# Performance work log

Hardware: AMD Instinct MI355X
Metric: run time of the kernel (lower is better)

## Reference

```python
import jax, jax.numpy as jnp
import numpy as np

USER_NUM = 100000
ITEM_NUM = 100000
N_NODES = USER_NUM + ITEM_NUM
EMB = 64
N_EDGES = 6400000
N_LAYERS = 3
LAYER_CL = 1
EPS = 0.1


def setup_inputs() -> dict:
    key = jax.random.key(0)
    k1, k2, k3, k4, k5, k6 = jax.random.split(key, 6)
    # Xavier-uniform-like scale for embeddings
    scale = float(np.sqrt(6.0 / (USER_NUM + EMB)))
    user_emb = jax.random.normal(k1, (USER_NUM, EMB), dtype=jnp.float32) * scale
    item_emb = jax.random.normal(k2, (ITEM_NUM, EMB), dtype=jnp.float32) * scale
    adj_rows = jax.random.randint(k3, (N_EDGES,), 0, N_NODES, dtype=jnp.int64)
    adj_cols = jax.random.randint(k4, (N_EDGES,), 0, N_NODES, dtype=jnp.int64)
    # normalized adjacency values ~ 1/degree
    adj_vals = jax.random.uniform(k5, (N_EDGES,), dtype=jnp.float32) * (1.0 / 32.0)
    # precomputed uniform noise replacing torch.rand_like per layer
    noise = jax.random.uniform(k6, (N_LAYERS, N_NODES, EMB), dtype=jnp.float32)
    return {"user_emb": user_emb, "item_emb": item_emb, "adj_rows": adj_rows,
            "adj_cols": adj_cols, "adj_vals": adj_vals, "noise": noise}


def _spmm(rows, cols, vals, x):
    # sparse [N,N] @ dense [N,D] via gather + segment_sum
    return jax.ops.segment_sum(vals[:, None] * x[cols], rows, num_segments=N_NODES)


def reference(user_emb, item_emb, adj_rows, adj_cols, adj_vals, noise):
    ego = jnp.concatenate([user_emb, item_emb], axis=0)  # [N, D]
    cl = ego
    acc = jnp.zeros_like(ego)
    for k in range(N_LAYERS):
        ego = _spmm(adj_rows, adj_cols, adj_vals, ego)
        # perturbed branch: ego += sign(ego) * F.normalize(noise_k, dim=-1) * eps
        nk = noise[k]
        nrm = jnp.maximum(jnp.linalg.norm(nk, axis=-1, keepdims=True), 1e-12)
        ego = ego + jnp.sign(ego) * (nk / nrm) * EPS
        acc = acc + ego
        if k == LAYER_CL - 1:
            cl = ego
    final = acc / N_LAYERS  # mean over stacked layer outputs
    return (final[:USER_NUM], final[USER_NUM:], cl[:USER_NUM], cl[USER_NUM:])
```

## Files before the change

kernel.cpp:

```cpp
#include <hip/hip_runtime.h>


#define USER_NUM 100000
#define N_NODES  200000
#define EMB      64
#define N_EDGES  6400000
#define NBUCK    782
#define CAP      9216
#define EPB      16384
#define TB_A     1024

static constexpr size_t BUFA_OFF  = 0;
static constexpr size_t BUFB_OFF  = 51200000;
static constexpr size_t CV_OFF    = 102400000;
static constexpr size_t RS_OFF    = 153600000;
static constexpr size_t SMALL_OFF = 154400016;
static constexpr size_t NRM_OFF   = 155200016;
static constexpr size_t WS_NEED   = 156000016;

__global__ __launch_bounds__(TB_A) void k_prep(const int* __restrict__ rows,
                                               const int* __restrict__ cols,
                                               const float* __restrict__ vals,
                                               int* __restrict__ bcnt,
                                               int2* __restrict__ zip) {
    __shared__ int h[NBUCK];
    for (int i = threadIdx.x; i < NBUCK; i += TB_A) h[i] = 0;
    __syncthreads();
    int base = blockIdx.x * EPB;
    int end  = min(base + EPB, N_EDGES);
    for (int e = base + threadIdx.x; e < end; e += TB_A) {
        atomicAdd(&h[rows[e] >> 8], 1);
        zip[e] = make_int2(cols[e], __float_as_int(vals[e]));
    }
    __syncthreads();
    for (int i = threadIdx.x; i < NBUCK; i += TB_A) {
        int c = h[i];
        if (c) atomicAdd(&bcnt[i], c);
    }
}

__global__ void k_scan782(const int* __restrict__ bcnt, int* __restrict__ bbase,
                          int* __restrict__ gcur, int* __restrict__ rs) {
    __shared__ int s[1024];
    int i = threadIdx.x;
    int v = (i < NBUCK) ? bcnt[i] : 0;
    s[i] = v;
    __syncthreads();
    for (int off = 1; off < 1024; off <<= 1) {
        int t = 0;
        if (i >= off) t = s[i - off];
        __syncthreads();
        s[i] += t;
        __syncthreads();
    }
    if (i < NBUCK) {
        int ex = s[i] - v;
        bbase[i] = ex;
        gcur[i] = ex;
    }
    if (i == 0) rs[N_NODES] = N_EDGES;
}

__global__ __launch_bounds__(TB_A) void k_bin(const int* __restrict__ rows,
                                              int* __restrict__ gcur,
                                              int* __restrict__ keys) {
    __shared__ int h[NBUCK];
    __shared__ int gb[NBUCK];
    for (int i = threadIdx.x; i < NBUCK; i += TB_A) h[i] = 0;
    __syncthreads();
    int base = blockIdx.x * EPB;
    int end  = min(base + EPB, N_EDGES);
    for (int e = base + threadIdx.x; e < end; e += TB_A)
        atomicAdd(&h[rows[e] >> 8], 1);
    __syncthreads();
    for (int i = threadIdx.x; i < NBUCK; i += TB_A) {
        int c = h[i];
        gb[i] = c ? atomicAdd(&gcur[i], c) : 0;
        h[i] = 0;
    }
    __syncthreads();
    for (int e = base + threadIdx.x; e < end; e += TB_A) {
        int r = rows[e];
        int b = r >> 8;
        int pos = gb[b] + atomicAdd(&h[b], 1);
        keys[pos] = ((r & 255) << 24) | e;
    }
}

__global__ __launch_bounds__(256) void k_build(const int* __restrict__ keys,
                                               const int2* __restrict__ zip,
                                               const int* __restrict__ bcnt,
                                               const int* __restrict__ bbase,
                                               int2* __restrict__ cv,
                                               int* __restrict__ rs) {
    __shared__ int cnt[256];
    __shared__ int start[256];
    __shared__ int cur[256];
    __shared__ int scanbuf[256];
    __shared__ int eKey[CAP];
    int tid = threadIdx.x;
    int b = blockIdx.x;
    int n = bcnt[b];
    int base = bbase[b];
    int rowbase = b << 8;
    cnt[tid] = 0;
    __syncthreads();
    for (int i = tid; i < n; i += 256) {
        unsigned key = (unsigned)keys[base + i];
        atomicAdd(&cnt[key >> 24], 1);
    }
    __syncthreads();
    int v = cnt[tid];
    scanbuf[tid] = v;
    __syncthreads();
    for (int off = 1; off < 256; off <<= 1) {
        int t = 0;
        if (tid >= off) t = scanbuf[tid - off];
        __syncthreads();
        scanbuf[tid] += t;
        __syncthreads();
    }
    start[tid] = scanbuf[tid] - v;
    {
        int row = rowbase + tid;
        if (row < N_NODES) rs[row] = base + start[tid];
    }
    cur[tid] = 0;
    __syncthreads();
    if (n <= CAP) {
        for (int i = tid; i < n; i += 256) {
            int key = keys[base + i];
            int rl = (int)((unsigned)key >> 24);
            int p = start[rl] + atomicAdd(&cur[rl], 1);
            eKey[p] = key;
        }
        __syncthreads();
        for (int p = tid; p < n; p += 256) {
            int k = eKey[p];
            int rl = (int)((unsigned)k >> 24);
            int s0 = start[rl];
            int s1 = s0 + cnt[rl];
            int rank = 0;
            int q = s0;
            for (; q + 4 <= s1; q += 4) {
                rank += (eKey[q]     < k);
                rank += (eKey[q + 1] < k);
                rank += (eKey[q + 2] < k);
                rank += (eKey[q + 3] < k);
            }
            for (; q < s1; ++q) rank += (eKey[q] < k);
            int e = k & 0x00FFFFFF;
            cv[base + s0 + rank] = zip[e];
        }
    } else {
        for (int i = tid; i < n; i += 256) {
            int key = keys[base + i];
            int rl = (int)((unsigned)key >> 24);
            int p = start[rl] + atomicAdd(&cur[rl], 1);
            cv[base + p] = make_int2(key, 0);
        }
        __syncthreads();
        int c = cnt[tid];
        if (c > 1) {
            int s0 = start[tid];
            int s1 = s0 + c;
            for (int i = s0 + 1; i < s1; ++i) {
                int2 kv = cv[base + i];
                int j = i - 1;
                while (j >= s0 && cv[base + j].x > kv.x) {
                    cv[base + j + 1] = cv[base + j];
                    --j;
                }
                cv[base + j + 1] = kv;
            }
        }
        __syncthreads();
        for (int i = tid; i < n; i += 256) {
            int e = cv[base + i].x & 0x00FFFFFF;
            cv[base + i] = zip[e];
        }
    }
}

__global__ void k_norm(const float* __restrict__ nk, float* __restrict__ nrm) {
    __shared__ float tile[2][64 * 65];
    int wave = threadIdx.x >> 6;
    int lane = threadIdx.x & 63;
    int base = blockIdx.x * 128 + wave * 64;
    for (int rr = 0; rr < 64; ++rr) {
        int row = base + rr;
        float v = 0.f;
        if (row < N_NODES) v = nk[row * EMB + lane];
        tile[wave][rr * 65 + lane] = v;
    }
    __syncthreads();
    int row = base + lane;
    if (row < N_NODES) {
        const float* tp = &tile[wave][lane * 65];
        float rj[8];
        #pragma unroll
        for (int j = 0; j < 8; ++j) {
            float xj = tp[j];
            rj[j] = __fmul_rn(xj, xj);
        }
        #pragma unroll
        for (int i = 8; i < 64; i += 8) {
            #pragma unroll
            for (int j = 0; j < 8; ++j) {
                float xj = tp[i + j];
                rj[j] = __fadd_rn(rj[j], __fmul_rn(xj, xj));
            }
        }
        float s01 = __fadd_rn(rj[0], rj[1]);
        float s23 = __fadd_rn(rj[2], rj[3]);
        float s45 = __fadd_rn(rj[4], rj[5]);
        float s67 = __fadd_rn(rj[6], rj[7]);
        float ss = __fadd_rn(__fadd_rn(s01, s23), __fadd_rn(s45, s67));
        float nv = __fsqrt_rn(ss);
        nv = fmaxf(nv, 1e-12f);
        nrm[row] = nv;
    }
}

__global__ __launch_bounds__(256) void k_fused(const int* __restrict__ rs,
                                               const int2* __restrict__ cv,
                                               const float* __restrict__ xlo,
                                               const float* __restrict__ xhi,
                                               int split,
                                               const float* __restrict__ nk,
                                               const float* __restrict__ nrm,
                                               float* __restrict__ ego,
                                               float* __restrict__ accF,
                                               float* __restrict__ clF,
                                               int mode) {
    int t = blockIdx.x * blockDim.x + threadIdx.x;
    if (t >= N_NODES * 16) return;
    int r = t >> 4;
    int c = (t & 15) << 2;
    int j0 = rs[r], j1 = rs[r + 1];
    float a0 = 0.f, a1 = 0.f, a2 = 0.f, a3 = 0.f;
    if (j0 < j1) {
        const int EMAX = N_EDGES - 1;
        #define XROW(col) (((col) < split ? xlo : xhi) + \
                           ((col) < split ? (col) : (col) - split) * EMB + c)
        int2 c0 = cv[j0];
        int2 c1 = cv[min(j0 + 1, EMAX)];
        int2 c2 = cv[min(j0 + 2, EMAX)];
        int2 n0 = cv[min(j0 + 3, EMAX)];
        int2 n1 = cv[min(j0 + 4, EMAX)];
        int2 n2 = cv[min(j0 + 5, EMAX)];
        int2 m0 = cv[min(j0 + 6, EMAX)];
        int2 m1 = cv[min(j0 + 7, EMAX)];
        int2 m2 = cv[min(j0 + 8, EMAX)];
        float4 x0 = *(const float4*)XROW(c0.x);
        float4 x1 = *(const float4*)XROW(c1.x);
        float4 x2 = *(const float4*)XROW(c2.x);
        for (int j = j0; j < j1; j += 3) {
            float4 y0 = *(const float4*)XROW(n0.x);
            float4 y1 = *(const float4*)XROW(n1.x);
            float4 y2 = *(const float4*)XROW(n2.x);
            float v0 = __int_as_float(c0.y);
            float v1 = (j + 1 < j1) ? __int_as_float(c1.y) : 0.f;
            float v2 = (j + 2 < j1) ? __int_as_float(c2.y) : 0.f;
            a0 = __fadd_rn(a0, __fmul_rn(v0, x0.x));
            a1 = __fadd_rn(a1, __fmul_rn(v0, x0.y));
            a2 = __fadd_rn(a2, __fmul_rn(v0, x0.z));
            a3 = __fadd_rn(a3, __fmul_rn(v0, x0.w));
            a0 = __fadd_rn(a0, __fmul_rn(v1, x1.x));
            a1 = __fadd_rn(a1, __fmul_rn(v1, x1.y));
            a2 = __fadd_rn(a2, __fmul_rn(v1, x1.z));
            a3 = __fadd_rn(a3, __fmul_rn(v1, x1.w));
            a0 = __fadd_rn(a0, __fmul_rn(v2, x2.x));
            a1 = __fadd_rn(a1, __fmul_rn(v2, x2.y));
            a2 = __fadd_rn(a2, __fmul_rn(v2, x2.z));
            a3 = __fadd_rn(a3, __fmul_rn(v2, x2.w));
            c0 = n0; c1 = n1; c2 = n2;
            n0 = m0; n1 = m1; n2 = m2;
            x0 = y0; x1 = y1; x2 = y2;
            m0 = cv[min(j + 9,  EMAX)];
            m1 = cv[min(j + 10, EMAX)];
            m2 = cv[min(j + 11, EMAX)];
        }
        #undef XROW
    }
    int idx = t << 2;
    float4 n4 = *(const float4*)(nk + idx);
    float nv = nrm[r];
    float4 e4;
    {
        float s, q;
        s = (a0 > 0.f) ? 1.f : ((a0 < 0.f) ? -1.f : 0.f);
        q = __fdiv_rn(n4.x, nv);
        e4.x = __fadd_rn(a0, __fmul_rn(__fmul_rn(s, q), 0.1f));
        s = (a1 > 0.f) ? 1.f : ((a1 < 0.f) ? -1.f : 0.f);
        q = __fdiv_rn(n4.y, nv);
        e4.y = __fadd_rn(a1, __fmul_rn(__fmul_rn(s, q), 0.1f));
        s = (a2 > 0.f) ? 1.f : ((a2 < 0.f) ? -1.f : 0.f);
        q = __fdiv_rn(n4.z, nv);
        e4.z = __fadd_rn(a2, __fmul_rn(__fmul_rn(s, q), 0.1f));
        s = (a3 > 0.f) ? 1.f : ((a3 < 0.f) ? -1.f : 0.f);
        q = __fdiv_rn(n4.w, nv);
        e4.w = __fadd_rn(a3, __fmul_rn(__fmul_rn(s, q), 0.1f));
    }
    if (mode == 0) {
        *(float4*)(ego + idx) = e4;
        *(float4*)(clF + idx) = e4;
    } else if (mode == 1) {
        *(float4*)(ego + idx) = e4;
        float4 a = *(const float4*)(clF + idx);
        a.x = __fadd_rn(a.x, e4.x);
        a.y = __fadd_rn(a.y, e4.y);
        a.z = __fadd_rn(a.z, e4.z);
        a.w = __fadd_rn(a.w, e4.w);
        *(float4*)(accF + idx) = a;
    } else {
        float4 a = *(const float4*)(accF + idx);
        float4 f;
        f.x = __fdiv_rn(__fadd_rn(a.x, e4.x), 3.0f);
        f.y = __fdiv_rn(__fadd_rn(a.y, e4.y), 3.0f);
        f.z = __fdiv_rn(__fadd_rn(a.z, e4.z), 3.0f);
        f.w = __fdiv_rn(__fadd_rn(a.w, e4.w), 3.0f);
        *(float4*)(accF + idx) = f;
    }
}

extern "C" void kernel_launch(void* const* d_in, const int* in_sizes, int n_in,
                              void* d_out, int out_size, void* d_ws, size_t ws_size,
                              hipStream_t stream) {
    if (ws_size < WS_NEED) return;

    const float* user_emb = (const float*)d_in[0];
    const float* item_emb = (const float*)d_in[1];
    const int*   adj_rows = (const int*)d_in[2];
    const int*   adj_cols = (const int*)d_in[3];
    const float* adj_vals = (const float*)d_in[4];
    const float* noise    = (const float*)d_in[5];

    char* ws = (char*)d_ws;
    float* bufA = (float*)(ws + BUFA_OFF);
    float* bufB = (float*)(ws + BUFB_OFF);
    int*   keys = (int*)(ws + BUFA_OFF);
    int2*  zip  = (int2*)(ws + BUFB_OFF);
    int2*  cv   = (int2*)(ws + CV_OFF);
    int*   rs   = (int*)(ws + RS_OFF);
    int*   bcnt = (int*)(ws + SMALL_OFF);
    int*   bbase= (int*)(ws + SMALL_OFF + 3200);
    int*   gcur = (int*)(ws + SMALL_OFF + 6400);
    float* nrm  = (float*)(ws + NRM_OFF);

    float* accF = (float*)d_out;
    float* clF  = (float*)d_out + (size_t)N_NODES * EMB;

    hipMemsetAsync(bcnt, 0, NBUCK * sizeof(int), stream);
    const int NBLK = (N_EDGES + EPB - 1) / EPB;
    k_prep<<<NBLK, TB_A, 0, stream>>>(adj_rows, adj_cols, adj_vals, bcnt, zip);
    k_scan782<<<1, 1024, 0, stream>>>(bcnt, bbase, gcur, rs);
    k_bin<<<NBLK, TB_A, 0, stream>>>(adj_rows, gcur, keys);
    k_build<<<NBUCK, 256, 0, stream>>>(keys, zip, bcnt, bbase, cv, rs);

    const int T16 = N_NODES * 16;
    for (int k = 0; k < 3; ++k) {
        const float* nkp = noise + (size_t)k * N_NODES * EMB;
        const float* xlo  = (k == 0) ? user_emb : ((k == 1) ? bufA : bufB);
        const float* xhi  = (k == 0) ? item_emb : ((k == 1) ? bufA : bufB);
        int split = (k == 0) ? USER_NUM : 0;
        float* ego_out = (k == 0) ? bufA : bufB;
        k_norm<<<(N_NODES + 127) / 128, 128, 0, stream>>>(nkp, nrm);
        k_fused<<<(T16 + 255) / 256, 256, 0, stream>>>(rs, cv, xlo, xhi, split,
                                                       nkp, nrm, ego_out, accF,
                                                       clF, k);
    }
}
```

Measured before the change: 1.406 ms.

## Fuse noise row-norm into SpMM kernel and replace bucket-count atomics with partials

```diff
diff --git a/kernel.cpp b/kernel.cpp
--- a/kernel.cpp
+++ b/kernel.cpp
@@ -9,6 +9,7 @@
 #define CAP      9216
 #define EPB      16384
 #define TB_A     1024
+#define NBLK     391
 
 static constexpr size_t BUFA_OFF  = 0;
 static constexpr size_t BUFB_OFF  = 51200000;
@@ -21,7 +22,7 @@
 __global__ __launch_bounds__(TB_A) void k_prep(const int* __restrict__ rows,
                                                const int* __restrict__ cols,
                                                const float* __restrict__ vals,
-                                               int* __restrict__ bcnt,
+                                               int* __restrict__ bcnt_part,
                                                int2* __restrict__ zip) {
     __shared__ int h[NBUCK];
     for (int i = threadIdx.x; i < NBUCK; i += TB_A) h[i] = 0;
@@ -33,17 +34,20 @@
         zip[e] = make_int2(cols[e], __float_as_int(vals[e]));
     }
     __syncthreads();
-    for (int i = threadIdx.x; i < NBUCK; i += TB_A) {
-        int c = h[i];
-        if (c) atomicAdd(&bcnt[i], c);
-    }
-}
-
-__global__ void k_scan782(const int* __restrict__ bcnt, int* __restrict__ bbase,
+    for (int i = threadIdx.x; i < NBUCK; i += TB_A)
+        bcnt_part[blockIdx.x * NBUCK + i] = h[i];
+}
+
+__global__ void k_scan782(const int* __restrict__ bcnt_part,
+                          int* __restrict__ bcnt, int* __restrict__ bbase,
                           int* __restrict__ gcur, int* __restrict__ rs) {
     __shared__ int s[1024];
     int i = threadIdx.x;
-    int v = (i < NBUCK) ? bcnt[i] : 0;
+    int v = 0;
+    if (i < NBUCK) {
+        for (int b = 0; b < NBLK; ++b) v += bcnt_part[b * NBUCK + i];
+        bcnt[i] = v;
+    }
     s[i] = v;
     __syncthreads();
     for (int off = 1; off < 1024; off <<= 1) {
@@ -182,61 +186,45 @@
     }
 }
 
-__global__ void k_norm(const float* __restrict__ nk, float* __restrict__ nrm) {
-    __shared__ float tile[2][64 * 65];
-    int wave = threadIdx.x >> 6;
-    int lane = threadIdx.x & 63;
-    int base = blockIdx.x * 128 + wave * 64;
-    for (int rr = 0; rr < 64; ++rr) {
-        int row = base + rr;
-        float v = 0.f;
-        if (row < N_NODES) v = nk[row * EMB + lane];
-        tile[wave][rr * 65 + lane] = v;
-    }
-    __syncthreads();
-    int row = base + lane;
-    if (row < N_NODES) {
-        const float* tp = &tile[wave][lane * 65];
-        float rj[8];
-        #pragma unroll
-        for (int j = 0; j < 8; ++j) {
-            float xj = tp[j];
-            rj[j] = __fmul_rn(xj, xj);
-        }
-        #pragma unroll
-        for (int i = 8; i < 64; i += 8) {
-            #pragma unroll
-            for (int j = 0; j < 8; ++j) {
-                float xj = tp[i + j];
-                rj[j] = __fadd_rn(rj[j], __fmul_rn(xj, xj));
-            }
-        }
-        float s01 = __fadd_rn(rj[0], rj[1]);
-        float s23 = __fadd_rn(rj[2], rj[3]);
-        float s45 = __fadd_rn(rj[4], rj[5]);
-        float s67 = __fadd_rn(rj[6], rj[7]);
-        float ss = __fadd_rn(__fadd_rn(s01, s23), __fadd_rn(s45, s67));
-        float nv = __fsqrt_rn(ss);
-        nv = fmaxf(nv, 1e-12f);
-        nrm[row] = nv;
-    }
-}
-
 __global__ __launch_bounds__(256) void k_fused(const int* __restrict__ rs,
                                                const int2* __restrict__ cv,
                                                const float* __restrict__ xlo,
                                                const float* __restrict__ xhi,
                                                int split,
                                                const float* __restrict__ nk,
-                                               const float* __restrict__ nrm,
                                                float* __restrict__ ego,
                                                float* __restrict__ accF,
                                                float* __restrict__ clF,
                                                int mode) {
     int t = blockIdx.x * blockDim.x + threadIdx.x;
-    if (t >= N_NODES * 16) return;
     int r = t >> 4;
-    int c = (t & 15) << 2;
+    int u = t & 15;
+    int c = u << 2;
+    int idx = t << 2;
+    float4 n4 = *(const float4*)(nk + idx);
+    float q0 = __fmul_rn(n4.x, n4.x);
+    float q1 = __fmul_rn(n4.y, n4.y);
+    float q2 = __fmul_rn(n4.z, n4.z);
+    float q3 = __fmul_rn(n4.w, n4.w);
+    float f0 = q0, f1 = q1, f2 = q2, f3 = q3;
+    #pragma unroll
+    for (int s = 0; s < 7; ++s) {
+        float g0 = __shfl_up(f0, 2, 16);
+        float g1 = __shfl_up(f1, 2, 16);
+        float g2 = __shfl_up(f2, 2, 16);
+        float g3 = __shfl_up(f3, 2, 16);
+        if (u >= 2) {
+            f0 = __fadd_rn(g0, q0);
+            f1 = __fadd_rn(g1, q1);
+            f2 = __fadd_rn(g2, q2);
+            f3 = __fadd_rn(g3, q3);
+        }
+    }
+    float tAB = __fadd_rn(__fadd_rn(f0, f1), __fadd_rn(f2, f3));
+    float tlo = __shfl(tAB, 14, 16);
+    float thi = __shfl(tAB, 15, 16);
+    float nv = __fsqrt_rn(__fadd_rn(tlo, thi));
+    nv = fmaxf(nv, 1e-12f);
     int j0 = rs[r], j1 = rs[r + 1];
     float a0 = 0.f, a1 = 0.f, a2 = 0.f, a3 = 0.f;
     if (j0 < j1) {
@@ -283,9 +271,6 @@
         }
         #undef XROW
     }
-    int idx = t << 2;
-    float4 n4 = *(const float4*)(nk + idx);
-    float nv = nrm[r];
     float4 e4;
     {
         float s, q;
@@ -341,20 +326,19 @@
     float* bufB = (float*)(ws + BUFB_OFF);
     int*   keys = (int*)(ws + BUFA_OFF);
     int2*  zip  = (int2*)(ws + BUFB_OFF);
+    int*   bcnt_part = (int*)(ws + CV_OFF);
     int2*  cv   = (int2*)(ws + CV_OFF);
     int*   rs   = (int*)(ws + RS_OFF);
     int*   bcnt = (int*)(ws + SMALL_OFF);
     int*   bbase= (int*)(ws + SMALL_OFF + 3200);
     int*   gcur = (int*)(ws + SMALL_OFF + 6400);
-    float* nrm  = (float*)(ws + NRM_OFF);
 
     float* accF = (float*)d_out;
     float* clF  = (float*)d_out + (size_t)N_NODES * EMB;
 
-    hipMemsetAsync(bcnt, 0, NBUCK * sizeof(int), stream);
-    const int NBLK = (N_EDGES + EPB - 1) / EPB;
-    k_prep<<<NBLK, TB_A, 0, stream>>>(adj_rows, adj_cols, adj_vals, bcnt, zip);
-    k_scan782<<<1, 1024, 0, stream>>>(bcnt, bbase, gcur, rs);
+    k_prep<<<NBLK, TB_A, 0, stream>>>(adj_rows, adj_cols, adj_vals, bcnt_part,
+                                      zip);
+    k_scan782<<<1, 1024, 0, stream>>>(bcnt_part, bcnt, bbase, gcur, rs);
     k_bin<<<NBLK, TB_A, 0, stream>>>(adj_rows, gcur, keys);
     k_build<<<NBUCK, 256, 0, stream>>>(keys, zip, bcnt, bbase, cv, rs);
 
@@ -365,9 +349,7 @@
         const float* xhi  = (k == 0) ? item_emb : ((k == 1) ? bufA : bufB);
         int split = (k == 0) ? USER_NUM : 0;
         float* ego_out = (k == 0) ? bufA : bufB;
-        k_norm<<<(N_NODES + 127) / 128, 128, 0, stream>>>(nkp, nrm);
-        k_fused<<<(T16 + 255) / 256, 256, 0, stream>>>(rs, cv, xlo, xhi, split,
-                                                       nkp, nrm, ego_out, accF,
-                                                       clF, k);
-    }
-}
+        k_fused<<<T16 / 256, 256, 0, stream>>>(rs, cv, xlo, xhi, split,
+                                               nkp, ego_out, accF, clF, k);
+    }
+}
```

After: 1.232 ms. -12.4%, faster.
